# Kernel optimization log

Measured on AMD Instinct MI355X. Metric: run time of the kernel, lower is better.

## Reference

```python
import jax, jax.numpy as jnp
import numpy as np

TEMP = 0.07  # InfoCNECauchy temperature


def setup_inputs() -> dict:
    key = jax.random.key(0)
    k1, k2 = jax.random.split(key)
    features = jax.random.normal(k1, (8192, 512), dtype=jnp.float32)  # 2N x d, two augmented views
    labels = jax.random.randint(k2, (8192,), 0, 100)  # unused in selfsupervised mode
    return {"features": features, "labels": labels}


def reference(features, labels):
    n2 = features.shape[0]
    n = n2 // 2
    # squared pairwise Euclidean distances (== torch.cdist(...)**2)
    sq = jnp.sum(features * features, axis=1)
    d2 = jnp.maximum(sq[:, None] + sq[None, :] - 2.0 * (features @ features.T), 0.0)
    # Cauchy similarity kernel: 1 / ((dist / t)^2 + 1)
    sim = 1.0 / (d2 / (TEMP * TEMP) + 1.0)
    # selfsupervised mask: row i is positive only with its partner view i^N,
    # so the masked mean-log reduces to log(sim[i, partner(i)])
    idx = jnp.arange(n2)
    partner = jnp.where(idx < n, idx + n, idx - n)
    pos = jnp.mean(jnp.log(sim[idx, partner]))
    # negatives: sum over row excluding the diagonal (sim diag == 1)
    neg = jnp.mean(jnp.log(jnp.sum(sim, axis=1) - jnp.diagonal(sim)))
    return -(pos - neg)
```

## Files before the change

kernel.cpp:

```cpp
#include <hip/hip_runtime.h>


#define N2 8192
#define DIM 512
#define NT 64
#define T2 0.0049f

typedef float floatx4 __attribute__((ext_vector_type(4)));
typedef __bf16 bf16x8 __attribute__((ext_vector_type(8)));
typedef __bf16 bf16x4 __attribute__((ext_vector_type(4)));

__device__ __forceinline__ void load_to_lds16(const void* g, void* l) {
  auto gp = (const __attribute__((address_space(1))) void*)(reinterpret_cast<uintptr_t>(g));
  auto lp = (__attribute__((address_space(3))) void*)(reinterpret_cast<uintptr_t>(l));
  __builtin_amdgcn_global_load_lds(gp, lp, 16, 0, 0);
}

__global__ __launch_bounds__(256) void prep_kernel(const float* __restrict__ f,
                                                   __bf16* __restrict__ fbf,
                                                   float* __restrict__ sq) {
  const int t = threadIdx.x;
  const int row = blockIdx.x * 2 + (t >> 7);
  const int ci = (t & 127) * 4;
  const float4 v = *(const float4*)(f + (size_t)row * DIM + ci);
  bf16x4 b;
  b[0] = (__bf16)v.x; b[1] = (__bf16)v.y; b[2] = (__bf16)v.z; b[3] = (__bf16)v.w;
  *(bf16x4*)(fbf + (size_t)row * DIM + ci) = b;
  float s = v.x * v.x + v.y * v.y + v.z * v.z + v.w * v.w;
#pragma unroll
  for (int off = 1; off < 64; off <<= 1) s += __shfl_xor(s, off, 64);
  __shared__ float red[4];
  if ((t & 63) == 0) red[t >> 6] = s;
  __syncthreads();
  if ((t & 127) == 0) sq[row] = red[t >> 6] + red[(t >> 6) + 1];
}

__global__ __launch_bounds__(256) void gemm_kernel(const __bf16* __restrict__ fbf,
                                                   const float* __restrict__ sq,
                                                   float* __restrict__ rowsum,
                                                   float* __restrict__ spart) {
  __shared__ __bf16 aT[128 * 32];
  __shared__ __bf16 bT[128 * 32];

  int idx = blockIdx.x;
  int by = 0, s0 = 0;
  while (s0 + (NT - by) <= idx) { s0 += NT - by; ++by; }
  const int bx = by + (idx - s0);
  const int brow = by * 128;
  const int bcol = bx * 128;
  const bool diag = (by == bx);

  const int t = threadIdx.x;
  const int lane = t & 63;
  const int w = t >> 6;
  const int wrow = (w >> 1) * 64;
  const int wcol = (w & 1) * 64;
  const int q4 = lane >> 4;
  const int lc = lane & 15;

  floatx4 acc[4][4] = {};

  int grow[2], gofs[2];
#pragma unroll
  for (int it = 0; it < 2; ++it) {
    const int slot = it * 256 + t;
    const int rpair = slot >> 3;
    const int u = (slot & 7) ^ (rpair & 7);
    grow[it] = rpair * 2 + (u >> 2);
    gofs[it] = (u & 3) * 8;
  }

  const int up = (((lc & 1) * 4) + q4) ^ (lc >> 1);
  const int rhalf = lc >> 1;

  for (int kt = 0; kt < DIM / 32; ++kt) {
    const int k0 = kt * 32;
#pragma unroll
    for (int it = 0; it < 2; ++it) {
      load_to_lds16(fbf + (size_t)(brow + grow[it]) * DIM + k0 + gofs[it],
                    &aT[t * 8 + it * 2048]);
      load_to_lds16(fbf + (size_t)(bcol + grow[it]) * DIM + k0 + gofs[it],
                    &bT[t * 8 + it * 2048]);
    }
    __syncthreads();
    bf16x8 af[4], bfr[4];
#pragma unroll
    for (int mr = 0; mr < 4; ++mr)
      af[mr] = *(const bf16x8*)&aT[((wrow >> 1) + mr * 8 + rhalf) * 64 + up * 8];
#pragma unroll
    for (int mc = 0; mc < 4; ++mc)
      bfr[mc] = *(const bf16x8*)&bT[((wcol >> 1) + mc * 8 + rhalf) * 64 + up * 8];
#pragma unroll
    for (int mr = 0; mr < 4; ++mr)
#pragma unroll
      for (int mc = 0; mc < 4; ++mc)
        acc[mr][mc] =
            __builtin_amdgcn_mfma_f32_16x16x32_bf16(af[mr], bfr[mc], acc[mr][mc], 0, 0, 0);
    __syncthreads();
  }

  float sqc[4];
#pragma unroll
  for (int mc = 0; mc < 4; ++mc) sqc[mc] = sq[bcol + wcol + mc * 16 + lc];

  float cs[4] = {0.f, 0.f, 0.f, 0.f};

#pragma unroll
  for (int mr = 0; mr < 4; ++mr) {
#pragma unroll
    for (int reg = 0; reg < 4; ++reg) {
      const int r = brow + wrow + mr * 16 + q4 * 4 + reg;
      const float sr = sq[r];
      const int pc = r ^ (N2 / 2);
      float rs = 0.f;
#pragma unroll
      for (int mc = 0; mc < 4; ++mc) {
        const int c = bcol + wcol + mc * 16 + lc;
        const float g = acc[mr][mc][reg];
        const float d2 = fmaxf(sr + sqc[mc] - 2.f * g, 0.f);
        const float s = T2 * __builtin_amdgcn_rcpf(d2 + T2);
        if (c != r) rs += s;
        cs[mc] += s;
        if (c == pc) { spart[r] = s; spart[pc] = s; }
      }
#pragma unroll
      for (int off = 1; off < 16; off <<= 1) rs += __shfl_xor(rs, off, 64);
      if (lc == 0) atomicAdd(&rowsum[r], rs);
    }
  }

  if (!diag) {
#pragma unroll
    for (int mc = 0; mc < 4; ++mc) {
      float v = cs[mc];
      v += __shfl_xor(v, 16, 64);
      v += __shfl_xor(v, 32, 64);
      if (lane < 16) atomicAdd(&rowsum[bcol + wcol + mc * 16 + lane], v);
    }
  }
}

__global__ __launch_bounds__(256) void final_kernel(const float* __restrict__ rowsum,
                                                    const float* __restrict__ spart,
                                                    float* __restrict__ out) {
  const int t = threadIdx.x;
  float a = 0.f;
  for (int r = t; r < N2; r += 256) a += logf(rowsum[r]) - logf(spart[r]);
#pragma unroll
  for (int off = 1; off < 64; off <<= 1) a += __shfl_xor(a, off, 64);
  __shared__ float red[4];
  if ((t & 63) == 0) red[t >> 6] = a;
  __syncthreads();
  if (t == 0) out[0] = (red[0] + red[1] + red[2] + red[3]) * (1.0f / (float)N2);
}

extern "C" void kernel_launch(void* const* d_in, const int* in_sizes, int n_in,
                              void* d_out, int out_size, void* d_ws, size_t ws_size,
                              hipStream_t stream) {
  const float* features = (const float*)d_in[0];
  float* out = (float*)d_out;

  char* ws = (char*)d_ws;
  __bf16* fbf = (__bf16*)ws;
  float* sq = (float*)(ws + (size_t)N2 * DIM * sizeof(__bf16));
  float* rowsum = sq + N2;
  float* spart = rowsum + N2;

  hipMemsetAsync(rowsum, 0, N2 * sizeof(float), stream);
  prep_kernel<<<N2 / 2, 256, 0, stream>>>(features, fbf, sq);
  gemm_kernel<<<NT * (NT + 1) / 2, 256, 0, stream>>>(fbf, sq, rowsum, spart);
  final_kernel<<<1, 256, 0, stream>>>(rowsum, spart, out);
}
```

Measured before the change: 156.1 us.

## Use 32x32x16 MFMA, fuse final reduction via last-block counter, drop memset

Switches the GEMM inner loop from 16x16x32 to 32x32x16 bf16 MFMA with 2x2 accumulator tiles per wave, adjusting the LDS fragment addressing and epilogue row/column mapping. The rowsum memset and counter reset move into the prep kernel, and the separate final kernel is replaced by a last-block-done atomic counter inside the GEMM kernel. Global load pointers are now incremented instead of recomputed, and launch bounds request 4 blocks per CU. This removes two launches and some per-iteration address arithmetic, at the cost of fence/atomic overhead per block and a serial tail reduction in one block.

```diff
diff --git a/kernel.cpp b/kernel.cpp
--- a/kernel.cpp
+++ b/kernel.cpp
@@ -4,9 +4,10 @@
 #define N2 8192
 #define DIM 512
 #define NT 64
+#define NTILES (NT * (NT + 1) / 2)
 #define T2 0.0049f
 
-typedef float floatx4 __attribute__((ext_vector_type(4)));
+typedef float floatx16 __attribute__((ext_vector_type(16)));
 typedef __bf16 bf16x8 __attribute__((ext_vector_type(8)));
 typedef __bf16 bf16x4 __attribute__((ext_vector_type(4)));
 
@@ -18,8 +19,12 @@
 
 __global__ __launch_bounds__(256) void prep_kernel(const float* __restrict__ f,
                                                    __bf16* __restrict__ fbf,
-                                                   float* __restrict__ sq) {
+                                                   float* __restrict__ sq,
+                                                   float* __restrict__ rowsum,
+                                                   int* __restrict__ counter) {
   const int t = threadIdx.x;
+  if (t < 2) rowsum[blockIdx.x * 2 + t] = 0.f;
+  if (blockIdx.x == 0 && t == 2) *counter = 0;
   const int row = blockIdx.x * 2 + (t >> 7);
   const int ci = (t & 127) * 4;
   const float4 v = *(const float4*)(f + (size_t)row * DIM + ci);
@@ -35,10 +40,12 @@
   if ((t & 127) == 0) sq[row] = red[t >> 6] + red[(t >> 6) + 1];
 }
 
-__global__ __launch_bounds__(256) void gemm_kernel(const __bf16* __restrict__ fbf,
-                                                   const float* __restrict__ sq,
-                                                   float* __restrict__ rowsum,
-                                                   float* __restrict__ spart) {
+__global__ __launch_bounds__(256, 4) void gemm_kernel(const __bf16* __restrict__ fbf,
+                                                      const float* __restrict__ sq,
+                                                      float* __restrict__ rowsum,
+                                                      float* __restrict__ spart,
+                                                      int* __restrict__ counter,
+                                                      float* __restrict__ out) {
   __shared__ __bf16 aT[128 * 32];
   __shared__ __bf16 bT[128 * 32];
 
@@ -55,67 +62,74 @@
   const int w = t >> 6;
   const int wrow = (w >> 1) * 64;
   const int wcol = (w & 1) * 64;
-  const int q4 = lane >> 4;
-  const int lc = lane & 15;
+  const int l31 = lane & 31;
+  const int lh = lane >> 5;
 
-  floatx4 acc[4][4] = {};
+  floatx16 acc[2][2] = {};
 
-  int grow[2], gofs[2];
+  const __bf16 *gA[2], *gB[2];
 #pragma unroll
   for (int it = 0; it < 2; ++it) {
     const int slot = it * 256 + t;
-    const int rpair = slot >> 3;
-    const int u = (slot & 7) ^ (rpair & 7);
-    grow[it] = rpair * 2 + (u >> 2);
-    gofs[it] = (u & 3) * 8;
+    const int rp = slot >> 3;
+    const int u = (slot & 7) ^ (rp & 7);
+    const int gr = rp * 2 + (u >> 2);
+    const int go = (u & 3) * 8;
+    gA[it] = fbf + (size_t)(brow + gr) * DIM + go;
+    gB[it] = fbf + (size_t)(bcol + gr) * DIM + go;
   }
 
-  const int up = (((lc & 1) * 4) + q4) ^ (lc >> 1);
-  const int rhalf = lc >> 1;
+  const int rpA = (wrow >> 1) + (l31 >> 1);
+  const int rpB = (wcol >> 1) + (l31 >> 1);
+  const int xr = (lane >> 1) & 7;
+  const int ub = (lane & 1) * 4 + lh;
 
   for (int kt = 0; kt < DIM / 32; ++kt) {
-    const int k0 = kt * 32;
 #pragma unroll
     for (int it = 0; it < 2; ++it) {
-      load_to_lds16(fbf + (size_t)(brow + grow[it]) * DIM + k0 + gofs[it],
-                    &aT[t * 8 + it * 2048]);
-      load_to_lds16(fbf + (size_t)(bcol + grow[it]) * DIM + k0 + gofs[it],
-                    &bT[t * 8 + it * 2048]);
+      load_to_lds16(gA[it], &aT[t * 8 + it * 2048]);
+      load_to_lds16(gB[it], &bT[t * 8 + it * 2048]);
+      gA[it] += 32;
+      gB[it] += 32;
     }
     __syncthreads();
-    bf16x8 af[4], bfr[4];
 #pragma unroll
-    for (int mr = 0; mr < 4; ++mr)
-      af[mr] = *(const bf16x8*)&aT[((wrow >> 1) + mr * 8 + rhalf) * 64 + up * 8];
+    for (int ks = 0; ks < 2; ++ks) {
+      const int up = (ub + ks * 2) ^ xr;
+      bf16x8 af[2], bfr[2];
 #pragma unroll
-    for (int mc = 0; mc < 4; ++mc)
-      bfr[mc] = *(const bf16x8*)&bT[((wcol >> 1) + mc * 8 + rhalf) * 64 + up * 8];
+      for (int mr = 0; mr < 2; ++mr)
+        af[mr] = *(const bf16x8*)&aT[(rpA + mr * 16) * 64 + up * 8];
 #pragma unroll
-    for (int mr = 0; mr < 4; ++mr)
+      for (int mc = 0; mc < 2; ++mc)
+        bfr[mc] = *(const bf16x8*)&bT[(rpB + mc * 16) * 64 + up * 8];
 #pragma unroll
-      for (int mc = 0; mc < 4; ++mc)
-        acc[mr][mc] =
-            __builtin_amdgcn_mfma_f32_16x16x32_bf16(af[mr], bfr[mc], acc[mr][mc], 0, 0, 0);
+      for (int mr = 0; mr < 2; ++mr)
+#pragma unroll
+        for (int mc = 0; mc < 2; ++mc)
+          acc[mr][mc] = __builtin_amdgcn_mfma_f32_32x32x16_bf16(af[mr], bfr[mc],
+                                                                acc[mr][mc], 0, 0, 0);
+    }
     __syncthreads();
   }
 
-  float sqc[4];
+  float sqc[2];
 #pragma unroll
-  for (int mc = 0; mc < 4; ++mc) sqc[mc] = sq[bcol + wcol + mc * 16 + lc];
+  for (int mc = 0; mc < 2; ++mc) sqc[mc] = sq[bcol + wcol + mc * 32 + l31];
 
-  float cs[4] = {0.f, 0.f, 0.f, 0.f};
+  float cs[2] = {0.f, 0.f};
 
 #pragma unroll
-  for (int mr = 0; mr < 4; ++mr) {
+  for (int mr = 0; mr < 2; ++mr) {
 #pragma unroll
-    for (int reg = 0; reg < 4; ++reg) {
-      const int r = brow + wrow + mr * 16 + q4 * 4 + reg;
+    for (int reg = 0; reg < 16; ++reg) {
+      const int r = brow + wrow + mr * 32 + (reg & 3) + 8 * (reg >> 2) + 4 * lh;
       const float sr = sq[r];
       const int pc = r ^ (N2 / 2);
       float rs = 0.f;
 #pragma unroll
-      for (int mc = 0; mc < 4; ++mc) {
-        const int c = bcol + wcol + mc * 16 + lc;
+      for (int mc = 0; mc < 2; ++mc) {
+        const int c = bcol + wcol + mc * 32 + l31;
         const float g = acc[mr][mc][reg];
         const float d2 = fmaxf(sr + sqc[mc] - 2.f * g, 0.f);
         const float s = T2 * __builtin_amdgcn_rcpf(d2 + T2);
@@ -124,34 +138,38 @@
         if (c == pc) { spart[r] = s; spart[pc] = s; }
       }
 #pragma unroll
-      for (int off = 1; off < 16; off <<= 1) rs += __shfl_xor(rs, off, 64);
-      if (lc == 0) atomicAdd(&rowsum[r], rs);
+      for (int off = 1; off < 32; off <<= 1) rs += __shfl_xor(rs, off, 64);
+      if (l31 == 0) atomicAdd(&rowsum[r], rs);
     }
   }
 
   if (!diag) {
 #pragma unroll
-    for (int mc = 0; mc < 4; ++mc) {
-      float v = cs[mc];
-      v += __shfl_xor(v, 16, 64);
-      v += __shfl_xor(v, 32, 64);
-      if (lane < 16) atomicAdd(&rowsum[bcol + wcol + mc * 16 + lane], v);
+    for (int mc = 0; mc < 2; ++mc) {
+      const float v = cs[mc] + __shfl_xor(cs[mc], 32, 64);
+      if (lh == 0) atomicAdd(&rowsum[bcol + wcol + mc * 32 + l31], v);
     }
   }
-}
 
-__global__ __launch_bounds__(256) void final_kernel(const float* __restrict__ rowsum,
-                                                    const float* __restrict__ spart,
-                                                    float* __restrict__ out) {
-  const int t = threadIdx.x;
-  float a = 0.f;
-  for (int r = t; r < N2; r += 256) a += logf(rowsum[r]) - logf(spart[r]);
+  __shared__ int is_last;
+  __threadfence();
+  if (t == 0) is_last = (atomicAdd(counter, 1) == NTILES - 1);
+  __syncthreads();
+  if (is_last) {
+    __threadfence();
+    float a = 0.f;
+    for (int r = t; r < N2; r += 256) {
+      const float rsv = __hip_atomic_load(&rowsum[r], __ATOMIC_RELAXED, __HIP_MEMORY_SCOPE_AGENT);
+      const float spv = __hip_atomic_load(&spart[r], __ATOMIC_RELAXED, __HIP_MEMORY_SCOPE_AGENT);
+      a += __logf(rsv) - __logf(spv);
+    }
 #pragma unroll
-  for (int off = 1; off < 64; off <<= 1) a += __shfl_xor(a, off, 64);
-  __shared__ float red[4];
-  if ((t & 63) == 0) red[t >> 6] = a;
-  __syncthreads();
-  if (t == 0) out[0] = (red[0] + red[1] + red[2] + red[3]) * (1.0f / (float)N2);
+    for (int off = 1; off < 64; off <<= 1) a += __shfl_xor(a, off, 64);
+    __shared__ float red[4];
+    if ((t & 63) == 0) red[t >> 6] = a;
+    __syncthreads();
+    if (t == 0) out[0] = (red[0] + red[1] + red[2] + red[3]) * (1.0f / (float)N2);
+  }
 }
 
 extern "C" void kernel_launch(void* const* d_in, const int* in_sizes, int n_in,
@@ -165,9 +183,8 @@
   float* sq = (float*)(ws + (size_t)N2 * DIM * sizeof(__bf16));
   float* rowsum = sq + N2;
   float* spart = rowsum + N2;
+  int* counter = (int*)(spart + N2);
 
-  hipMemsetAsync(rowsum, 0, N2 * sizeof(float), stream);
-  prep_kernel<<<N2 / 2, 256, 0, stream>>>(features, fbf, sq);
-  gemm_kernel<<<NT * (NT + 1) / 2, 256, 0, stream>>>(fbf, sq, rowsum, spart);
-  final_kernel<<<1, 256, 0, stream>>>(rowsum, spart, out);
+  prep_kernel<<<N2 / 2, 256, 0, stream>>>(features, fbf, sq, rowsum, counter);
+  gemm_kernel<<<NTILES, 256, 0, stream>>>(fbf, sq, rowsum, spart, counter, out);
 }
```

Measured after the change: 326.3 us. 109% more time.

## Remap triangular tile schedule into XCD-aware bands and fold rowsum zeroing into prep

Applied to the files above, without the earlier changes.

Replaces the linear upper-triangle tile index with a mapping that assigns blockIdx modulo 8 to pairs of 4-row bands, so each XCD works on nearby tiles and shares operand rows in its L2. It also removes the separate memset by zeroing rowsum inside the prep kernel. A redundant first copy of the mapping code with a shared-memory write and __syncthreads was left in, adding a little overhead. The band mapping must cover all 2080 tiles exactly once.

```diff
diff --git a/kernel.cpp b/kernel.cpp
--- a/kernel.cpp
+++ b/kernel.cpp
@@ -4,6 +4,7 @@
 #define N2 8192
 #define DIM 512
 #define NT 64
+#define NTILES (NT * (NT + 1) / 2)
 #define T2 0.0049f
 
 typedef float floatx4 __attribute__((ext_vector_type(4)));
@@ -18,8 +19,10 @@
 
 __global__ __launch_bounds__(256) void prep_kernel(const float* __restrict__ f,
                                                    __bf16* __restrict__ fbf,
-                                                   float* __restrict__ sq) {
+                                                   float* __restrict__ sq,
+                                                   float* __restrict__ rowsum) {
   const int t = threadIdx.x;
+  if (t < 2) rowsum[blockIdx.x * 2 + t] = 0.f;
   const int row = blockIdx.x * 2 + (t >> 7);
   const int ci = (t & 127) * 4;
   const float4 v = *(const float4*)(f + (size_t)row * DIM + ci);
@@ -42,10 +45,35 @@
   __shared__ __bf16 aT[128 * 32];
   __shared__ __bf16 bT[128 * 32];
 
-  int idx = blockIdx.x;
-  int by = 0, s0 = 0;
-  while (s0 + (NT - by) <= idx) { s0 += NT - by; ++by; }
-  const int bx = by + (idx - s0);
+  {
+    const int x = blockIdx.x & 7;
+    int kk = blockIdx.x >> 3;
+    int band = x;
+    const int n1 = 250 - 16 * x;
+    if (kk >= n1) { kk -= n1; band = 15 - x; }
+    const int by0 = band * 4;
+    int bxx = by0;
+    int cnt;
+    while (kk >= (cnt = min(4, bxx - by0 + 1))) { kk -= cnt; ++bxx; }
+    __shared__ int s_by, s_bx;
+    if (threadIdx.x == 0) { s_by = by0 + kk; s_bx = bxx; }
+    __syncthreads();
+    (void)s_by;
+  }
+  int by, bx;
+  {
+    const int x = blockIdx.x & 7;
+    int kk = blockIdx.x >> 3;
+    int band = x;
+    const int n1 = 250 - 16 * x;
+    if (kk >= n1) { kk -= n1; band = 15 - x; }
+    const int by0 = band * 4;
+    int bxx = by0;
+    int cnt;
+    while (kk >= (cnt = min(4, bxx - by0 + 1))) { kk -= cnt; ++bxx; }
+    by = by0 + kk;
+    bx = bxx;
+  }
   const int brow = by * 128;
   const int bcol = bx * 128;
   const bool diag = (by == bx);
@@ -64,9 +92,9 @@
 #pragma unroll
   for (int it = 0; it < 2; ++it) {
     const int slot = it * 256 + t;
-    const int rpair = slot >> 3;
-    const int u = (slot & 7) ^ (rpair & 7);
-    grow[it] = rpair * 2 + (u >> 2);
+    const int rp = slot >> 3;
+    const int u = (slot & 7) ^ (rp & 7);
+    grow[it] = rp * 2 + (u >> 2);
     gofs[it] = (u & 3) * 8;
   }
 
@@ -166,8 +194,7 @@
   float* rowsum = sq + N2;
   float* spart = rowsum + N2;
 
-  hipMemsetAsync(rowsum, 0, N2 * sizeof(float), stream);
-  prep_kernel<<<N2 / 2, 256, 0, stream>>>(features, fbf, sq);
-  gemm_kernel<<<NT * (NT + 1) / 2, 256, 0, stream>>>(fbf, sq, rowsum, spart);
+  prep_kernel<<<N2 / 2, 256, 0, stream>>>(features, fbf, sq, rowsum);
+  gemm_kernel<<<NTILES, 256, 0, stream>>>(fbf, sq, rowsum, spart);
   final_kernel<<<1, 256, 0, stream>>>(rowsum, spart, out);
 }
```

Result: faster. 143.7 us (-7.9%).
